# Performance work log

Measured on AMD Instinct MI355X. Metric: run time of the kernel, lower is better.

## Reference

```python
import jax, jax.numpy as jnp
import numpy as np

N_USERS, N_ITEMS = 6000, 4000
EPS = 1e-8


def _cosine_similarity(X):
    # rows of X normalized to unit length, then dense gram matrix [n, n]
    norms = jnp.linalg.norm(X, axis=1, keepdims=True) + EPS
    Xn = X / norms
    return Xn @ Xn.T


def _top_k_adjacency(S, k):
    # faithful, vectorized version of the per-row Python loop in the torch code:
    # take top-(k+1), drop the self index, keep the first k remaining entries,
    # scatter values into a sparse-pattern adjacency, then symmetrize.
    n = S.shape[0]
    k_actual = min(k + 1, n)
    vals, idx = jax.lax.top_k(S, k_actual)          # [n, k+1]
    rows = jnp.arange(n)[:, None]                    # [n, 1]
    valid = idx != rows                              # exclude self
    # keep only the first k valid entries per row ( [:k] truncation in torch )
    keep = valid & (jnp.cumsum(valid, axis=1) <= k)
    vals = jnp.where(keep, vals, 0.0)
    adj = jnp.zeros_like(S).at[rows, idx].set(vals)  # indices distinct per row
    return (adj + adj.T) * 0.5


def _sym_normalize(A):
    row_sums = A.sum(axis=1, keepdims=True) + EPS
    col_sums = A.sum(axis=0, keepdims=True) + EPS
    return A / jnp.sqrt(row_sums) / jnp.sqrt(col_sums)


def setup_inputs() -> dict:
    key = jax.random.key(0)
    R = jax.random.uniform(key, (N_USERS, N_ITEMS), dtype=jnp.float32)
    return {"R": R, "k_users": 50, "k_items": 20}


def reference(R, k_users, k_items):
    # user-user graph from cosine similarity over interaction rows
    user_adj = _sym_normalize(_top_k_adjacency(_cosine_similarity(R), k_users))
    # item-item graph from cosine similarity over interaction columns
    item_adj = _sym_normalize(_top_k_adjacency(_cosine_similarity(R.T), k_items))
    # two-sided spectral-style propagation of the interaction signal
    out = user_adj @ (R @ item_adj)                  # [n_users, n_items]
    return out
```

## Files before the change

### kernel.cpp

```cpp
#include <hip/hip_runtime.h>
#include <math.h>

#define EPS 1e-8f

constexpr int N_USERS = 6000;
constexpr int N_ITEMS = 4000;
constexpr int NU_P = 6016;
constexpr int NI_P = 4096;

typedef __bf16 bf16_8 __attribute__((ext_vector_type(8)));
typedef float f32_4 __attribute__((ext_vector_type(4)));
typedef int i32x4 __attribute__((ext_vector_type(4)));

__device__ __forceinline__ void stage16(const void* g, void* l) {
  __builtin_amdgcn_global_load_lds(
      (const __attribute__((address_space(1))) void*)g,
      (__attribute__((address_space(3))) void*)l, 16, 0, 0);
}

__device__ __forceinline__ int xcd_swz(int p, int nwg) {
  return (p & 7) * (nwg >> 3) + (p >> 3);
}

__device__ __forceinline__ void tri_decode(int p, int& by, int& bx) {
  int r = (int)((sqrtf(8.f * p + 1.f) - 1.f) * 0.5f);
  while ((r + 1) * (r + 2) / 2 <= p) r++;
  while (r * (r + 1) / 2 > p) r--;
  by = r;
  bx = p - r * (r + 1) / 2;
}

__device__ __forceinline__ void grp_decode(int p, int nby, int nbx, int& by,
                                           int& bx) {
  const int G = 8;
  const int wide = G * nbx;
  const int band = p / wide;
  const int rem = p - band * wide;
  const int h = min(G, nby - band * G);
  by = band * G + rem % h;
  bx = rem / h;
}

template <int KK, int LDA, int LDB, int LDC, int OUTBF16>
__global__ __launch_bounds__(256) void mfma_prop_bf16(
    const __bf16* __restrict__ A, const __bf16* __restrict__ B,
    float* __restrict__ Cf, __bf16* __restrict__ Cb, int M, int N, int nby,
    int nbx) {
  __shared__ __bf16 sA[2][128 * 32];
  __shared__ __bf16 sB[2][128 * 32];

  int by, bx;
  grp_decode(xcd_swz(blockIdx.x, gridDim.x), nby, nbx, by, bx);

  const int tid = threadIdx.x;
  const int lane = tid & 63;
  const int wave = tid >> 6;
  const int wm = (wave >> 1) * 64;
  const int wn = (wave & 1) * 64;
  const int lm = lane & 15;
  const int kg = lane >> 4;
  const long row0 = (long)by * 128;
  const long col0 = (long)bx * 128;

  f32_4 acc[4][4];
#pragma unroll
  for (int i = 0; i < 4; i++)
#pragma unroll
    for (int j = 0; j < 4; j++) acc[i][j] = (f32_4){0.f, 0.f, 0.f, 0.f};

  const int c0 = tid, c1 = tid + 256;
  const int r0c = c0 >> 2, j0c = ((c0 & 3) - (r0c >> 1)) & 3;
  const int r1c = c1 >> 2, j1c = ((c1 & 3) - (r1c >> 1)) & 3;

  int offA[4], offB[4];
#pragma unroll
  for (int i = 0; i < 4; i++) {
    const int ra = wm + i * 16 + lm;
    const int rb = wn + i * 16 + lm;
    offA[i] = (ra * 4 + ((kg + (ra >> 1)) & 3)) * 8;
    offB[i] = (rb * 4 + ((kg + (rb >> 1)) & 3)) * 8;
  }

  const __bf16* a0 = A + (row0 + r0c) * LDA + j0c * 8;
  const __bf16* a1 = A + (row0 + r1c) * LDA + j1c * 8;
  const __bf16* b0 = B + (col0 + r0c) * LDB + j0c * 8;
  const __bf16* b1 = B + (col0 + r1c) * LDB + j1c * 8;

  for (int k0 = 0; k0 < KK; k0 += 64) {
    stage16(a0 + k0, &sA[0][c0 * 8]);
    stage16(a1 + k0, &sA[0][c1 * 8]);
    stage16(b0 + k0, &sB[0][c0 * 8]);
    stage16(b1 + k0, &sB[0][c1 * 8]);
    stage16(a0 + k0 + 32, &sA[1][c0 * 8]);
    stage16(a1 + k0 + 32, &sA[1][c1 * 8]);
    stage16(b0 + k0 + 32, &sB[1][c0 * 8]);
    stage16(b1 + k0 + 32, &sB[1][c1 * 8]);
    __syncthreads();

#pragma unroll
    for (int h = 0; h < 2; h++) {
      bf16_8 a[4], b[4];
#pragma unroll
      for (int i = 0; i < 4; i++) {
        a[i] = *(const bf16_8*)&sA[h][offA[i]];
        b[i] = *(const bf16_8*)&sB[h][offB[i]];
      }
#pragma unroll
      for (int i = 0; i < 4; i++)
#pragma unroll
        for (int j = 0; j < 4; j++)
          acc[i][j] = __builtin_amdgcn_mfma_f32_16x16x32_bf16(a[i], b[j],
                                                              acc[i][j], 0, 0,
                                                              0);
    }
    __syncthreads();
  }

#pragma unroll
  for (int i = 0; i < 4; i++)
#pragma unroll
    for (int j = 0; j < 4; j++)
#pragma unroll
      for (int r = 0; r < 4; r++) {
        const long gm = row0 + wm + i * 16 + kg * 4 + r;
        const long gn = col0 + wn + j * 16 + lm;
        if (gm < M && gn < N) {
          if (OUTBF16)
            Cb[gm * LDC + gn] = (__bf16)acc[i][j][r];
          else
            Cf[gm * LDC + gn] = acc[i][j][r];
        }
      }
}

template <int KK, int LD, int LDC>
__global__ __launch_bounds__(256) void mfma_gram_i8(
    const signed char* __restrict__ Q, const float* __restrict__ sv,
    float* __restrict__ C, int Nn, float negq) {
  __shared__ signed char sA[128 * 64];
  __shared__ signed char sB[128 * 64];

  int by, bx;
  tri_decode(xcd_swz(blockIdx.x, gridDim.x), by, bx);

  const int tid = threadIdx.x;
  const int lane = tid & 63;
  const int wave = tid >> 6;
  const int wm = (wave >> 1) * 64;
  const int wn = (wave & 1) * 64;
  const int lm = lane & 15;
  const int kg = lane >> 4;
  const long row0 = (long)by * 128;
  const long col0 = (long)bx * 128;
  const float scale = 1.f / (254.f * 254.f);

  i32x4 acc[4][4];
#pragma unroll
  for (int i = 0; i < 4; i++)
#pragma unroll
    for (int j = 0; j < 4; j++) acc[i][j] = (i32x4){0, 0, 0, 0};

  const int c0 = tid, c1 = tid + 256;
  const int r0c = c0 >> 2, j0c = ((c0 & 3) - (r0c >> 1)) & 3;
  const int r1c = c1 >> 2, j1c = ((c1 & 3) - (r1c >> 1)) & 3;

  int offA[4], offB[4];
#pragma unroll
  for (int i = 0; i < 4; i++) {
    const int ra = wm + i * 16 + lm;
    const int rb = wn + i * 16 + lm;
    offA[i] = (ra * 4 + ((kg + (ra >> 1)) & 3)) * 16;
    offB[i] = (rb * 4 + ((kg + (rb >> 1)) & 3)) * 16;
  }

  const signed char* a0 = Q + (row0 + r0c) * LD + j0c * 16;
  const signed char* a1 = Q + (row0 + r1c) * LD + j1c * 16;
  const signed char* b0 = Q + (col0 + r0c) * LD + j0c * 16;
  const signed char* b1 = Q + (col0 + r1c) * LD + j1c * 16;

  for (int k0 = 0; k0 < KK; k0 += 64) {
    stage16(a0 + k0, &sA[c0 * 16]);
    stage16(a1 + k0, &sA[c1 * 16]);
    stage16(b0 + k0, &sB[c0 * 16]);
    stage16(b1 + k0, &sB[c1 * 16]);
    __syncthreads();

    i32x4 a[4], b[4];
#pragma unroll
    for (int i = 0; i < 4; i++) {
      a[i] = *(const i32x4*)&sA[offA[i]];
      b[i] = *(const i32x4*)&sB[offB[i]];
    }
#pragma unroll
    for (int i = 0; i < 4; i++)
#pragma unroll
      for (int j = 0; j < 4; j++)
        acc[i][j] = __builtin_amdgcn_mfma_i32_16x16x64_i8(a[i], b[j],
                                                          acc[i][j], 0, 0, 0);
    __syncthreads();
  }

#pragma unroll
  for (int i = 0; i < 4; i++)
#pragma unroll
    for (int j = 0; j < 4; j++)
#pragma unroll
      for (int r = 0; r < 4; r++) {
        const long gm = row0 + wm + i * 16 + kg * 4 + r;
        const long gn = col0 + wn + j * 16 + lm;
        if (gm < Nn && gn < Nn)
          C[gm * LDC + gn] = fmaf((float)acc[i][j][r], scale,
                                  0.5f * (sv[gm] + sv[gn]) + negq);
      }
}

__global__ __launch_bounds__(256) void pad_quant_kernel(
    const float* __restrict__ R, __bf16* __restrict__ H,
    signed char* __restrict__ Qp, int M, int N, int Np) {
  const int r = blockIdx.y;
  const int c = blockIdx.x * 256 + threadIdx.x;
  if (c >= Np) return;
  const bool in = (r < M && c < N);
  const float v = in ? R[(long)r * N + c] : 0.f;
  H[(long)r * Np + c] = (__bf16)v;
  Qp[(long)r * Np + c] =
      in ? (signed char)__float2int_rn((v - 0.5f) * 254.f) : (signed char)0;
}

__global__ __launch_bounds__(256) void transpose_quant_kernel(
    const float* __restrict__ R, signed char* __restrict__ Qp, int M, int N,
    int Mp, int Np) {
  __shared__ float tile[32][33];
  const int tx = threadIdx.x & 31;
  const int ty = threadIdx.x >> 5;
  const int ri = blockIdx.y * 32;
  const int ci = blockIdx.x * 32;
#pragma unroll
  for (int k = 0; k < 4; k++) {
    const int r = ri + ty + k * 8, c = ci + tx;
    tile[ty + k * 8][tx] = (r < M && c < N) ? R[(long)r * N + c] : 0.f;
  }
  __syncthreads();
#pragma unroll
  for (int k = 0; k < 4; k++) {
    const int orow = ci + ty + k * 8;
    const int ocol = ri + tx;
    if (orow < Np && ocol < Mp) {
      const bool in = (orow < N && ocol < M);
      const float v = tile[tx][ty + k * 8];
      Qp[(long)orow * Mp + ocol] =
          in ? (signed char)__float2int_rn((v - 0.5f) * 254.f) : (signed char)0;
    }
  }
}

__global__ __launch_bounds__(256) void mirror_kernel(float* __restrict__ S,
                                                     int n) {
  __shared__ float tile[32][33];
  int by, bx;
  tri_decode(blockIdx.x, by, bx);
  const int tj = by + 1, ti = bx;
  const int sr = tj * 32, sc = ti * 32;
  const int tx = threadIdx.x & 31;
  const int ty = threadIdx.x >> 5;
#pragma unroll
  for (int k = 0; k < 4; k++) {
    const int r = sr + ty + k * 8, c = sc + tx;
    tile[ty + k * 8][tx] = (r < n && c < n) ? S[(long)r * n + c] : 0.f;
  }
  __syncthreads();
#pragma unroll
  for (int k = 0; k < 4; k++) {
    const int r = sc + ty + k * 8, c = sr + tx;
    if (r < n && c < n) S[(long)r * n + c] = tile[tx][ty + k * 8];
  }
}

__global__ __launch_bounds__(256) void row_norm_sum(
    const float* __restrict__ R, float* __restrict__ inv_n,
    float* __restrict__ sv, int M, int K) {
  __shared__ float redA[256];
  __shared__ float redB[256];
  const int row = blockIdx.x;
  float s2 = 0.f, s1 = 0.f;
  for (int j = threadIdx.x; j < K; j += 256) {
    const float v = R[(long)row * K + j];
    s2 = fmaf(v, v, s2);
    s1 += v;
  }
  redA[threadIdx.x] = s2;
  redB[threadIdx.x] = s1;
  __syncthreads();
  for (int o = 128; o > 0; o >>= 1) {
    if (threadIdx.x < o) {
      redA[threadIdx.x] += redA[threadIdx.x + o];
      redB[threadIdx.x] += redB[threadIdx.x + o];
    }
    __syncthreads();
  }
  if (threadIdx.x == 0) {
    inv_n[row] = 1.f / (sqrtf(redA[0]) + EPS);
    sv[row] = redB[0];
  }
}

__global__ __launch_bounds__(256) void col_sums_kernel(
    const float* __restrict__ R, float* __restrict__ acc2,
    float* __restrict__ acc1, int M, int N, int rows_per_chunk) {
  const int j = blockIdx.x * 256 + threadIdx.x;
  if (j >= N) return;
  const int r0 = blockIdx.y * rows_per_chunk;
  const int r1 = min(M, r0 + rows_per_chunk);
  float s2 = 0.f, s1 = 0.f;
  for (int i = r0; i < r1; i++) {
    const float v = R[(long)i * N + j];
    s2 = fmaf(v, v, s2);
    s1 += v;
  }
  atomicAdd(&acc2[j], s2);
  atomicAdd(&acc1[j], s1);
}

__global__ __launch_bounds__(256) void inv_norm_finalize(
    const float* __restrict__ acc, float* __restrict__ inv_n, int n) {
  const int i = blockIdx.x * 256 + threadIdx.x;
  if (i < n) inv_n[i] = 1.f / (sqrtf(acc[i]) + EPS);
}

__global__ __launch_bounds__(64) void topk_kernel(
    float* __restrict__ G, const float* __restrict__ inv_n,
    __bf16* __restrict__ adj, float* __restrict__ rowsum,
    float* __restrict__ colsum, int n, int np, const int* __restrict__ kptr) {
  const int row = blockIdx.x;
  const int lane = threadIdx.x;
  const int k = *kptr;
  const float invr = inv_n[row];

  float v0 = -INFINITY, v1 = -INFINITY, v2 = -INFINITY, v3 = -INFINITY;
  int i0 = n, i1 = n, i2 = n, i3 = n;

  for (int j = lane; j < n; j += 64) {
    const float v =
        (j == row) ? -INFINITY : G[(long)row * n + j] * invr * inv_n[j];
    if (v > v3) {
      if (v > v1) {
        if (v > v0) {
          v3 = v2; i3 = i2; v2 = v1; i2 = i1; v1 = v0; i1 = i0; v0 = v; i0 = j;
        } else {
          v3 = v2; i3 = i2; v2 = v1; i2 = i1; v1 = v; i1 = j;
        }
      } else {
        if (v > v2) {
          v3 = v2; i3 = i2; v2 = v; i2 = j;
        } else {
          v3 = v; i3 = j;
        }
      }
    }
  }

  float rsum = 0.f;
  for (int t = 0; t < k; t++) {
    float v = v0;
    int i = i0;
#pragma unroll
    for (int off = 32; off > 0; off >>= 1) {
      const float ov = __shfl_xor(v, off);
      const int oi = __shfl_xor(i, off);
      if (ov > v || (ov == v && oi < i)) { v = ov; i = oi; }
    }
    if (lane == 0) {
      adj[(long)row * np + i] = (__bf16)v;
      atomicAdd(&colsum[i], v);
      rsum += v;
    }
    if ((i & 63) == lane) {
      G[(long)row * n + i] = -INFINITY;
      v0 = v1; i0 = i1; v1 = v2; i1 = i2; v2 = v3; i2 = i3;
      v3 = -INFINITY; i3 = n;
      if (i0 == n) {
        for (int j = lane; j < n; j += 64) {
          const float vv =
              (j == row) ? -INFINITY : G[(long)row * n + j] * invr * inv_n[j];
          if (vv > v3) {
            if (vv > v1) {
              if (vv > v0) {
                v3 = v2; i3 = i2; v2 = v1; i2 = i1; v1 = v0; i1 = i0;
                v0 = vv; i0 = j;
              } else {
                v3 = v2; i3 = i2; v2 = v1; i2 = i1; v1 = vv; i1 = j;
              }
            } else {
              if (vv > v2) {
                v3 = v2; i3 = i2; v2 = vv; i2 = j;
              } else {
                v3 = vv; i3 = j;
              }
            }
          }
        }
      }
    }
  }
  if (lane == 0) rowsum[row] = rsum;
}

__global__ __launch_bounds__(256) void finalize_kernel(
    const float* __restrict__ rs, const float* __restrict__ cs,
    float* __restrict__ f, int n) {
  const int i = blockIdx.x * 256 + threadIdx.x;
  if (i < n) f[i] = rsqrtf(0.5f * (rs[i] + cs[i]) + EPS);
}

__global__ __launch_bounds__(256) void symscale_kernel(
    __bf16* __restrict__ adj, const float* __restrict__ f, int n, int np) {
  const int i = blockIdx.y;
  const int j = blockIdx.x * 256 + threadIdx.x;
  if (j >= np || j <= i || i >= n || j >= n) return;
  const float a = (float)adj[(long)i * np + j];
  const float b = (float)adj[(long)j * np + i];
  const float m = 0.5f * (a + b) * f[i] * f[j];
  adj[(long)i * np + j] = (__bf16)m;
  adj[(long)j * np + i] = (__bf16)m;
}

extern "C" void kernel_launch(void* const* d_in, const int* in_sizes, int n_in,
                              void* d_out, int out_size, void* d_ws,
                              size_t ws_size, hipStream_t stream) {
  const float* R = (const float*)d_in[0];
  const int* k_users_p = (const int*)d_in[1];
  const int* k_items_p = (const int*)d_in[2];
  float* out = (float*)d_out;
  const int NU = N_USERS, NI = N_ITEMS;

  char* ws = (char*)d_ws;
  float* invNu = (float*)(ws + 0);
  float* invNi = (float*)(ws + 32768);
  float* rsU = (float*)(ws + 65536);
  float* csU = (float*)(ws + 98304);
  float* rsI = (float*)(ws + 131072);
  float* csI = (float*)(ws + 163840);
  float* fU = (float*)(ws + 196608);
  float* fI = (float*)(ws + 229376);
  float* nrmI = (float*)(ws + 262144);
  float* svU = (float*)(ws + 294912);
  float* svI = (float*)(ws + 327680);
  const long MB = 1000000L;
  __bf16* Rh = (__bf16*)(ws + 1 * MB);
  signed char* Uh = (signed char*)(ws + 51 * MB);
  float* Su = (float*)(ws + 77 * MB);
  signed char* IhT = (signed char*)(ws + 103 * MB);
  float* Si = (float*)(ws + 128 * MB);
  __bf16* adjIb = (__bf16*)(ws + 222 * MB);
  __bf16* adjUb = (__bf16*)(ws + 256 * MB);
  __bf16* Tt = (__bf16*)(ws + 77 * MB);

  row_norm_sum<<<NU, 256, 0, stream>>>(R, invNu, svU, NU, NI);
  hipMemsetAsync(nrmI, 0, NI * sizeof(float), stream);
  hipMemsetAsync(svI, 0, NI * sizeof(float), stream);
  col_sums_kernel<<<dim3((NI + 255) / 256, 60), 256, 0, stream>>>(R, nrmI, svI,
                                                                  NU, NI, 100);
  inv_norm_finalize<<<(NI + 255) / 256, 256, 0, stream>>>(nrmI, invNi, NI);
  pad_quant_kernel<<<dim3(NI_P / 256, NU_P), 256, 0, stream>>>(R, Rh, Uh, NU,
                                                               NI, NI_P);
  transpose_quant_kernel<<<dim3(NI_P / 32, NU_P / 32), 256, 0, stream>>>(
      R, IhT, NU, NI, NU_P, NI_P);

  mfma_gram_i8<NU_P, NU_P, N_ITEMS><<<32 * 33 / 2, 256, 0, stream>>>(
      IhT, svI, Si, NI, -0.25f * (float)NU);
  {
    const int T = (NI + 31) / 32;
    mirror_kernel<<<T * (T - 1) / 2, 256, 0, stream>>>(Si, NI);
  }
  hipMemsetAsync(adjIb, 0, (long)NI_P * NI_P * sizeof(__bf16), stream);
  hipMemsetAsync(csI, 0, NI * sizeof(float), stream);
  topk_kernel<<<NI, 64, 0, stream>>>(Si, invNi, adjIb, rsI, csI, NI, NI_P,
                                     k_items_p);
  finalize_kernel<<<(NI + 255) / 256, 256, 0, stream>>>(rsI, csI, fI, NI);
  symscale_kernel<<<dim3((NI_P + 255) / 256, NI_P), 256, 0, stream>>>(
      adjIb, fI, NI, NI_P);

  mfma_gram_i8<NI_P, NI_P, N_USERS><<<47 * 48 / 2, 256, 0, stream>>>(
      Uh, svU, Su, NU, -0.25f * (float)NI);
  {
    const int T = (NU + 31) / 32;
    mirror_kernel<<<T * (T - 1) / 2, 256, 0, stream>>>(Su, NU);
  }
  hipMemsetAsync(adjUb, 0, (long)NU_P * NU_P * sizeof(__bf16), stream);
  hipMemsetAsync(csU, 0, NU * sizeof(float), stream);
  topk_kernel<<<NU, 64, 0, stream>>>(Su, invNu, adjUb, rsU, csU, NU, NU_P,
                                     k_users_p);
  finalize_kernel<<<(NU + 255) / 256, 256, 0, stream>>>(rsU, csU, fU, NU);
  symscale_kernel<<<dim3((NU_P + 255) / 256, NU_P), 256, 0, stream>>>(
      adjUb, fU, NU, NU_P);

  mfma_prop_bf16<NI_P, NI_P, NI_P, NU_P, 1><<<32 * 47, 256, 0, stream>>>(
      adjIb, Rh, nullptr, Tt, NI_P, NU_P, 32, 47);
  mfma_prop_bf16<NU_P, NU_P, NU_P, N_ITEMS, 0><<<47 * 32, 256, 0, stream>>>(
      adjUb, Tt, out, nullptr, NU, NI, 47, 32);
}
```

Before: 1.711 ms.

## Replace dense item-adjacency propagation GEMM with compacted sparse SpMM

```diff
diff --git a/kernel.cpp b/kernel.cpp
--- a/kernel.cpp
+++ b/kernel.cpp
@@ -7,6 +7,7 @@
 constexpr int N_ITEMS = 4000;
 constexpr int NU_P = 6016;
 constexpr int NI_P = 4096;
+constexpr int CMP_W = 192;
 
 typedef __bf16 bf16_8 __attribute__((ext_vector_type(8)));
 typedef float f32_4 __attribute__((ext_vector_type(4)));
@@ -214,15 +215,103 @@
       }
 }
 
+__global__ __launch_bounds__(256) void compact_adj_kernel(
+    const __bf16* __restrict__ adj, unsigned int* __restrict__ lists,
+    int* __restrict__ cnts, float* __restrict__ rsw, int n, int np) {
+  __shared__ int cnt;
+  __shared__ float sum;
+  const int i = blockIdx.x;
+  if (threadIdx.x == 0) {
+    cnt = 0;
+    sum = 0.f;
+  }
+  __syncthreads();
+  float my = 0.f;
+  for (int j = threadIdx.x; j < n; j += 256) {
+    const __bf16 a = adj[(long)i * np + j];
+    const float av = (float)a;
+    if (av != 0.f) {
+      const int slot = atomicAdd(&cnt, 1);
+      if (slot < CMP_W) {
+        const unsigned short bits = *(const unsigned short*)&a;
+        lists[(long)i * CMP_W + slot] =
+            ((unsigned int)bits << 16) | (unsigned int)j;
+      }
+      my += av;
+    }
+  }
+  atomicAdd(&sum, my);
+  __syncthreads();
+  if (threadIdx.x == 0) {
+    cnts[i] = min(cnt, CMP_W);
+    rsw[i] = sum;
+  }
+}
+
+__global__ __launch_bounds__(256) void spmm_prop1_kernel(
+    const unsigned int* __restrict__ lists, const int* __restrict__ cnts,
+    const float* __restrict__ rsw, const signed char* __restrict__ Qt,
+    __bf16* __restrict__ Tt) {
+  __shared__ unsigned int L[CMP_W];
+  __shared__ int scnt;
+  __shared__ float srs;
+  const int i = blockIdx.x;
+  const int t = threadIdx.x;
+  if (t == 0) {
+    scnt = cnts[i];
+    srs = rsw[i];
+  }
+  if (t < CMP_W) L[t] = lists[(long)i * CMP_W + t];
+  __syncthreads();
+  const int cnt = scnt;
+
+  float acc[6][4];
+#pragma unroll
+  for (int s = 0; s < 6; s++)
+#pragma unroll
+    for (int q = 0; q < 4; q++) acc[s][q] = 0.f;
+
+  for (int e = 0; e < cnt; e++) {
+    const unsigned int pk = L[e];
+    const unsigned short wb = (unsigned short)(pk >> 16);
+    const float w = (float)(*(const __bf16*)&wb);
+    const long jrow = (long)(pk & 0xffffu) * NU_P;
+#pragma unroll
+    for (int s = 0; s < 6; s++) {
+      const int u0 = 4 * t + 1024 * s;
+      if (u0 < NU_P) {
+        const char4 q4 = *(const char4*)&Qt[jrow + u0];
+        acc[s][0] = fmaf(w, (float)q4.x, acc[s][0]);
+        acc[s][1] = fmaf(w, (float)q4.y, acc[s][1]);
+        acc[s][2] = fmaf(w, (float)q4.z, acc[s][2]);
+        acc[s][3] = fmaf(w, (float)q4.w, acc[s][3]);
+      }
+    }
+  }
+
+  const float base = 0.5f * srs;
+  const long orow = (long)i * NU_P;
+#pragma unroll
+  for (int s = 0; s < 6; s++) {
+    const int u0 = 4 * t + 1024 * s;
+    if (u0 < NU_P) {
+      __bf16 o4[4];
+#pragma unroll
+      for (int q = 0; q < 4; q++)
+        o4[q] = (__bf16)fmaf(acc[s][q], 1.f / 254.f, base);
+      *(uint2*)&Tt[orow + u0] = *(const uint2*)&o4[0];
+    }
+  }
+}
+
 __global__ __launch_bounds__(256) void pad_quant_kernel(
-    const float* __restrict__ R, __bf16* __restrict__ H,
-    signed char* __restrict__ Qp, int M, int N, int Np) {
+    const float* __restrict__ R, signed char* __restrict__ Qp, int M, int N,
+    int Np) {
   const int r = blockIdx.y;
   const int c = blockIdx.x * 256 + threadIdx.x;
   if (c >= Np) return;
   const bool in = (r < M && c < N);
   const float v = in ? R[(long)r * N + c] : 0.f;
-  H[(long)r * Np + c] = (__bf16)v;
   Qp[(long)r * Np + c] =
       in ? (signed char)__float2int_rn((v - 0.5f) * 254.f) : (signed char)0;
 }
@@ -446,10 +535,12 @@
   float* svU = (float*)(ws + 294912);
   float* svI = (float*)(ws + 327680);
   const long MB = 1000000L;
-  __bf16* Rh = (__bf16*)(ws + 1 * MB);
+  signed char* IhT = (signed char*)(ws + 1 * MB);
+  unsigned int* cmpL = (unsigned int*)(ws + 26 * MB);
+  int* cmpC = (int*)(ws + 29500000L);
+  float* cmpR = (float*)(ws + 29700000L);
   signed char* Uh = (signed char*)(ws + 51 * MB);
   float* Su = (float*)(ws + 77 * MB);
-  signed char* IhT = (signed char*)(ws + 103 * MB);
   float* Si = (float*)(ws + 128 * MB);
   __bf16* adjIb = (__bf16*)(ws + 222 * MB);
   __bf16* adjUb = (__bf16*)(ws + 256 * MB);
@@ -461,8 +552,8 @@
   col_sums_kernel<<<dim3((NI + 255) / 256, 60), 256, 0, stream>>>(R, nrmI, svI,
                                                                   NU, NI, 100);
   inv_norm_finalize<<<(NI + 255) / 256, 256, 0, stream>>>(nrmI, invNi, NI);
-  pad_quant_kernel<<<dim3(NI_P / 256, NU_P), 256, 0, stream>>>(R, Rh, Uh, NU,
-                                                               NI, NI_P);
+  pad_quant_kernel<<<dim3(NI_P / 256, NU_P), 256, 0, stream>>>(R, Uh, NU, NI,
+                                                               NI_P);
   transpose_quant_kernel<<<dim3(NI_P / 32, NU_P / 32), 256, 0, stream>>>(
       R, IhT, NU, NI, NU_P, NI_P);
 
@@ -479,6 +570,8 @@
   finalize_kernel<<<(NI + 255) / 256, 256, 0, stream>>>(rsI, csI, fI, NI);
   symscale_kernel<<<dim3((NI_P + 255) / 256, NI_P), 256, 0, stream>>>(
       adjIb, fI, NI, NI_P);
+  compact_adj_kernel<<<NI, 256, 0, stream>>>(adjIb, cmpL, cmpC, cmpR, NI,
+                                             NI_P);
 
   mfma_gram_i8<NI_P, NI_P, N_USERS><<<47 * 48 / 2, 256, 0, stream>>>(
       Uh, svU, Su, NU, -0.25f * (float)NI);
@@ -494,8 +587,9 @@
   symscale_kernel<<<dim3((NU_P + 255) / 256, NU_P), 256, 0, stream>>>(
       adjUb, fU, NU, NU_P);
 
-  mfma_prop_bf16<NI_P, NI_P, NI_P, NU_P, 1><<<32 * 47, 256, 0, stream>>>(
-      adjIb, Rh, nullptr, Tt, NI_P, NU_P, 32, 47);
+  hipMemsetAsync(Tt + (long)NI * NU_P, 0,
+                 (long)(NI_P - NI) * NU_P * sizeof(__bf16), stream);
+  spmm_prop1_kernel<<<NI, 256, 0, stream>>>(cmpL, cmpC, cmpR, IhT, Tt);
   mfma_prop_bf16<NU_P, NU_P, NU_P, N_ITEMS, 0><<<47 * 32, 256, 0, stream>>>(
       adjUb, Tt, out, nullptr, NU, NI, 47, 32);
 }
```

Result: slower. 1.746 ms (+2.0%).
